# Optimization experiments

Measured on AMD Instinct MI355X. Metric: run time of the kernel, lower is better.

## Reference

```python
import jax, jax.numpy as jnp
import numpy as np

B, T, D, H, OUT = 64, 2048, 40, 164, 7


def _lstm_layer(xs, lengths, W_ih, W_hh, b):
    """xs: [T,B,Din] -> (all hiddens [T,B,H], last valid hidden [B,H]).

    Matches packed-sequence semantics: state stops updating once t >= length,
    so the final carry h equals the hidden at each sequence's last real step.
    PyTorch gate order: i, f, g, o.
    """
    Tt, Bb, _ = xs.shape
    gx = jnp.einsum('tbd,gd->tbg', xs, W_ih) + b  # input projections, one big GEMM

    def step(carry, inp):
        h, c = carry
        g_t, t = inp
        gates = g_t + h @ W_hh.T
        i, f, g, o = jnp.split(gates, 4, axis=-1)
        c_new = jax.nn.sigmoid(f) * c + jax.nn.sigmoid(i) * jnp.tanh(g)
        h_new = jax.nn.sigmoid(o) * jnp.tanh(c_new)
        m = (t < lengths)[:, None]  # freeze state past each sequence's length
        return (jnp.where(m, h_new, h), jnp.where(m, c_new, c)), jnp.where(m, h_new, h)

    z = jnp.zeros((Bb, W_hh.shape[1]), xs.dtype)
    (hT, _), hs = jax.lax.scan(step, (z, z), (gx, jnp.arange(Tt)))
    return hs, hT


def setup_inputs() -> dict:
    key = jax.random.key(0)
    ks = jax.random.split(key, 16)
    s = 1.0 / np.sqrt(H)
    inp = {
        'x': jax.random.normal(ks[0], (B, T, D), jnp.float32),
        'lengths': jax.random.randint(ks[1], (B,), 1, T + 1, jnp.int32),
        'W_ih_0': jax.random.normal(ks[2], (4 * H, D), jnp.float32) * s,
        'W_hh_0': jax.random.normal(ks[3], (4 * H, H), jnp.float32) * s,
        'b_0': jax.random.normal(ks[4], (4 * H,), jnp.float32) * s,
        'W_ih_1': jax.random.normal(ks[5], (4 * H, H), jnp.float32) * s,
        'W_hh_1': jax.random.normal(ks[6], (4 * H, H), jnp.float32) * s,
        'b_1': jax.random.normal(ks[7], (4 * H,), jnp.float32) * s,
        'W_ih_2': jax.random.normal(ks[8], (4 * H, H), jnp.float32) * s,
        'W_hh_2': jax.random.normal(ks[9], (4 * H, H), jnp.float32) * s,
        'b_2': jax.random.normal(ks[10], (4 * H,), jnp.float32) * s,
        'fc_w': jax.random.normal(ks[11], (OUT, H), jnp.float32) * s,
        'fc_b': jax.random.normal(ks[12], (OUT,), jnp.float32) * s,
    }
    return inp


def reference(x, lengths, W_ih_0, W_hh_0, b_0, W_ih_1, W_hh_1, b_1,
              W_ih_2, W_hh_2, b_2, fc_w, fc_b):
    xs = jnp.swapaxes(x, 0, 1)  # [T,B,D] for time-major scan
    hs, _ = _lstm_layer(xs, lengths, W_ih_0, W_hh_0, b_0)
    hs, _ = _lstm_layer(hs, lengths, W_ih_1, W_hh_1, b_1)
    _, hT = _lstm_layer(hs, lengths, W_ih_2, W_hh_2, b_2)  # hidden[-1]
    return hT @ fc_w.T + fc_b  # [B, OUT]
```

## Files before the change

### kernel.cpp

```cpp
#include <hip/hip_runtime.h>
#include <stdint.h>


#define TT 2048
#define BB 64
#define GG 656
#define HH 164
#define EP 176
#define GP 704
#define KPH 192
#define KPD 96
#define CC 64
#define NCH (TT/CC)
#define TSL 8
#define NSL (CC/TSL)
#define GEMM_BLKS (3*4*NSL)
#define REC_BLKS  48

typedef _Float16 half2v __attribute__((ext_vector_type(2)));
typedef _Float16 half8  __attribute__((ext_vector_type(8)));
typedef float    f32x4  __attribute__((ext_vector_type(4)));

#define SZ_WIH   ((size_t)3*GG*KPH*2)
#define SZ_WHH   ((size_t)3*GP*KPH*2)
#define SZ_GX1   ((size_t)3*16*CC*GG*4*2)
#define GX_SLOT_HALVES ((size_t)3*16*CC*GG*4)
#define SZ_HR    ((size_t)2*2*BB*CC*96*4)
#define HR_DW    (2*2*BB*CC*96)
#define SZ_SC    ((size_t)3*BB*HH*4)
#define SZ_SH    ((size_t)3*BB*96*4)

#define LOG2E 1.4426950408889634f

__device__ __forceinline__ float fexp2(float x) {
#if __has_builtin(__builtin_amdgcn_exp2f)
  return __builtin_amdgcn_exp2f(x);
#else
  float r; asm("v_exp_f32 %0, %1" : "=v"(r) : "v"(x)); return r;
#endif
}
__device__ __forceinline__ float frcp(float x) {
#if __has_builtin(__builtin_amdgcn_rcpf)
  return __builtin_amdgcn_rcpf(x);
#else
  float r; asm("v_rcp_f32 %0, %1" : "=v"(r) : "v"(x)); return r;
#endif
}
__device__ __forceinline__ float sigmf(float x) {
  return frcp(1.0f + fexp2(-LOG2E * x));
}
__device__ __forceinline__ float tanhf_(float x) {
  return __builtin_fmaf(-2.0f, frcp(1.0f + fexp2(2.0f * LOG2E * x)), 1.0f);
}

__global__ void kprep_w(const float* wih0, const float* whh0,
                        const float* wih1, const float* whh1,
                        const float* wih2, const float* whh2,
                        _Float16* wih16, _Float16* whh16) {
  int i = threadIdx.x + blockIdx.x * blockDim.x;
  if (i >= 3*GP*KPH) return;
  int l = i / (GP*KPH);
  int r2 = i - l*(GP*KPH);
  int prow = r2 / KPH;
  int k = r2 - prow*KPH;
  const float* wihl = (l == 0) ? wih0 : ((l == 1) ? wih1 : wih2);
  const float* whhl = (l == 0) ? whh0 : ((l == 1) ? whh1 : whh2);
  int g = prow / EP, e = prow - g*EP;
  float vh = 0.f;
  if (e < HH && k < HH) vh = whhl[(size_t)(g*HH + e)*HH + k];
  whh16[((size_t)l*GP + prow)*KPH + k] = (_Float16)vh;
  if (prow < GG) {
    float vi = 0.f;
    if (l == 0) { if (k < 40) vi = wihl[(size_t)prow*40 + k]; }
    else        { if (k < HH) vi = wihl[(size_t)prow*HH + k]; }
    wih16[((size_t)l*GG + prow)*KPH + k] = (_Float16)vi;
  }
}

__global__ void kzero(uint32_t* p, int n) {
  int i = threadIdx.x + blockIdx.x * blockDim.x;
  if (i < n) p[i] = 0u;
}

__device__ __forceinline__ void gemm_body(
    int l, int bg, int ts, int ch, const int* lengths, const float* x,
    const uint32_t* wihw, const uint32_t* hring, const float* bp,
    uint16_t* gxs, uint32_t* smem, int tid) {
  int maxlen = 1;
  #pragma unroll
  for (int bi = 0; bi < 16; ++bi) {
    int L = lengths[bg*16 + bi]; if (L < 1) L = 1; if (L > TT) L = TT;
    if (L > maxlen) maxlen = L;
  }
  const int tb = ts*TSL;
  const int t0 = ch*CC + tb;
  if (t0 >= maxlen) return;
  int tcnt = maxlen - t0; if (tcnt > TSL) tcnt = TSL;

  if (l == 0) {
    for (int idx = tid; idx < TSL*16*96; idx += 704) {
      int tloc = idx / 1536, r = idx - tloc*1536, b = r / 96, dw = r - b*96;
      uint32_t v = 0;
      if (dw < 20) {
        const float* xs = x + ((size_t)(bg*16 + b)*TT + (t0 + tloc))*40 + dw*2;
        half2v pp; pp[0] = (_Float16)xs[0]; pp[1] = (_Float16)xs[1];
        v = __builtin_bit_cast(uint32_t, pp);
      }
      smem[(tloc*16 + b)*100 + dw] = v;
    }
  } else {
    const uint32_t* hbs = hring + ((size_t)((l-1)*2 + (ch & 1))*BB)*CC*96;
    for (int idx = tid; idx < TSL*16*96; idx += 704) {
      int tloc = idx / 1536, r = idx - tloc*1536, b = r / 96, dw = r - b*96;
      smem[(tloc*16 + b)*100 + dw] =
          hbs[((size_t)(bg*16 + b)*CC + tb + tloc)*96 + dw];
    }
  }
  __syncthreads();

  const int lane = tid & 63, wv = tid >> 6;
  const int quad = lane >> 4, n15 = lane & 15;
  uint16_t* gxo = gxs + (((size_t)(l*16 + bg*4 + quad)*CC + tb)*GG)*4;

  half8 wf[4][6];
  float bv[4] = {0.f, 0.f, 0.f, 0.f};
  #pragma unroll
  for (int ni = 0; ni < 4; ++ni) {
    int nt = wv + ni*11;
    if (nt < 41) {
      int wrow = nt*16 + n15;
      const half8* bsrc = (const half8*)(wihw + ((size_t)l*GG + wrow)*KPD);
      #pragma unroll
      for (int kk = 0; kk < 6; ++kk) wf[ni][kk] = bsrc[kk*4 + quad];
      bv[ni] = bp[wrow];
    }
  }

  for (int tloc = 0; tloc < tcnt; ++tloc) {
    const half8* asrc = (const half8*)(smem + tloc*1600);
    half8 af[6];
    #pragma unroll
    for (int kk = 0; kk < 6; ++kk) af[kk] = asrc[n15*25 + kk*4 + quad];
    #pragma unroll
    for (int ni = 0; ni < 4; ++ni) {
      int nt = wv + ni*11;
      if (nt < 41) {
        int wrow = nt*16 + n15;
        f32x4 a0 = {0.f,0.f,0.f,0.f};
        #pragma unroll
        for (int kk = 0; kk < 6; ++kk)
          a0 = __builtin_amdgcn_mfma_f32_16x16x32_f16(af[kk], wf[ni][kk], a0, 0, 0, 0);
        half2v p0; p0[0] = (_Float16)(a0[0] + bv[ni]); p0[1] = (_Float16)(a0[1] + bv[ni]);
        half2v p1; p1[0] = (_Float16)(a0[2] + bv[ni]); p1[1] = (_Float16)(a0[3] + bv[ni]);
        uint2 pk;
        pk.x = __builtin_bit_cast(uint32_t, p0);
        pk.y = __builtin_bit_cast(uint32_t, p1);
        *(uint2*)(gxo + ((size_t)tloc*GG + wrow)*4) = pk;
      }
    }
  }
}

__device__ __forceinline__ void rec_body(
    int l, int bg, int ch, const int* lengths,
    const uint32_t* whhw, const uint16_t* gxs, uint32_t* hring,
    float* state_c, uint32_t* state_h, uint32_t* smem, int tid) {

  const int gb0 = bg*4;
  int maxlen = 1;
  #pragma unroll
  for (int bi = 0; bi < 4; ++bi) {
    int L = lengths[gb0 + bi]; if (L < 1) L = 1; if (L > TT) L = TT;
    if (L > maxlen) maxlen = L;
  }
  const int t0 = ch*CC;
  if (t0 >= maxlen) return;
  int t1 = t0 + CC; if (t1 > maxlen) t1 = maxlen;
  const int nst = t1 - t0;

  const int wv = tid >> 6, ln = tid & 63;
  const int quad = ln >> 4, n15 = ln & 15;
  const int e = wv*16 + n15;
  const int evalid = (e < HH);
  const int gb = gb0 + quad;

  int lenq = lengths[gb]; if (lenq < 1) lenq = 1; if (lenq > TT) lenq = TT;

  half8 wB[24];
  {
    const half8* wb8 = (const half8*)(whhw + (size_t)l*GP*KPD);
    #pragma unroll
    for (int g = 0; g < 4; ++g) {
      int row = g*EP + e;
      #pragma unroll
      for (int kk = 0; kk < 6; ++kk)
        wB[g*6 + kk] = wb8[(size_t)row*24 + kk*4 + quad];
    }
  }

  float creg = 0.f;
  if (ch > 0 && evalid)
    creg = state_c[((size_t)l*BB + gb)*HH + e];

  uint32_t* hb0 = smem;
  uint32_t* hb1 = smem + 1600;
  for (int i2 = tid; i2 < 1600; i2 += 704) {
    int bb = i2 / 100, dd = i2 - bb*100;
    uint32_t v = 0;
    if (dd < 96 && ch > 0) v = state_h[((size_t)l*BB + gb0 + (bb >> 2))*96 + dd];
    hb0[i2] = v; hb1[i2] = v;
  }
  __syncthreads();

  uint16_t hbit = ((const uint16_t*)hb0)[(quad*4)*200 + e];

  const uint16_t* gpt = gxs + (((size_t)(l*16 + bg)*CC)*GG)*4
                            + (size_t)e*4 + quad;
  uint16_t gxv[4];
  #pragma unroll
  for (int g = 0; g < 4; ++g) gxv[g] = gpt[g*(HH*4)];
  gpt += GG*4;

  const int dorb = (l < 2);
  uint16_t* rp;
  {
    uint16_t* hrb16 = (uint16_t*)(hring + ((size_t)(l*2 + (ch & 1))*BB)*CC*96);
    rp = hrb16 + ((size_t)gb*CC)*192 + e;
  }

  const int lo = n15*100 + quad*4;
  const int ho_off = (quad*4)*200 + e;

  int p = 0;
  for (int it = 0; it < nst; ++it) {
    const int t = t0 + it;
    uint32_t* hin  = p ? hb1 : hb0;
    uint32_t* hout = p ? hb0 : hb1;

    float gxf0 = (float)__builtin_bit_cast(_Float16, gxv[0]);
    float gxf1 = (float)__builtin_bit_cast(_Float16, gxv[1]);
    float gxf2 = (float)__builtin_bit_cast(_Float16, gxv[2]);
    float gxf3 = (float)__builtin_bit_cast(_Float16, gxv[3]);
    #pragma unroll
    for (int g = 0; g < 4; ++g) gxv[g] = gpt[g*(HH*4)];
    gpt += GG*4;

    f32x4 acc0, acc1, acc2, acc3;
    {
      const f32x4 z = {0.f, 0.f, 0.f, 0.f};
      half8 af = *(const half8*)&hin[lo];
      acc0 = __builtin_amdgcn_mfma_f32_16x16x32_f16(af, wB[0],  z, 0, 0, 0);
      acc1 = __builtin_amdgcn_mfma_f32_16x16x32_f16(af, wB[6],  z, 0, 0, 0);
      acc2 = __builtin_amdgcn_mfma_f32_16x16x32_f16(af, wB[12], z, 0, 0, 0);
      acc3 = __builtin_amdgcn_mfma_f32_16x16x32_f16(af, wB[18], z, 0, 0, 0);
    }
    #pragma unroll
    for (int kk = 1; kk < 6; ++kk) {
      half8 af = *(const half8*)&hin[lo + kk*16];
      acc0 = __builtin_amdgcn_mfma_f32_16x16x32_f16(af, wB[kk],      acc0, 0, 0, 0);
      acc1 = __builtin_amdgcn_mfma_f32_16x16x32_f16(af, wB[6 + kk],  acc1, 0, 0, 0);
      acc2 = __builtin_amdgcn_mfma_f32_16x16x32_f16(af, wB[12 + kk], acc2, 0, 0, 0);
      acc3 = __builtin_amdgcn_mfma_f32_16x16x32_f16(af, wB[18 + kk], acc3, 0, 0, 0);
    }
    {
      float gi = acc0[0] + gxf0;
      float gf = acc1[0] + gxf1;
      float gg2 = acc2[0] + gxf2;
      float go = acc3[0] + gxf3;
      float cn = sigmf(gf)*creg + sigmf(gi)*tanhf_(gg2);
      float hv = sigmf(go)*tanhf_(cn);
      if (t < lenq) {
        creg = cn;
        _Float16 h16 = (_Float16)hv;
        hbit = __builtin_bit_cast(uint16_t, h16);
      }
      if (evalid) {
        ((uint16_t*)hout)[ho_off] = hbit;
        if (dorb) *rp = hbit;
      }
      rp += 192;
    }
    asm volatile("s_waitcnt lgkmcnt(0)" ::: "memory");
    __builtin_amdgcn_s_barrier();
    p ^= 1;
  }

  uint32_t* hfin = p ? hb1 : hb0;
  uint32_t* shb = state_h + ((size_t)l*BB + gb0)*96;
  for (int i2 = tid; i2 < 4*96; i2 += 704) {
    int bb = i2 / 96, dd = i2 - bb*96;
    shb[(size_t)bb*96 + dd] = hfin[(bb*4)*100 + dd];
  }
  if (evalid)
    state_c[((size_t)l*BB + gb)*HH + e] = creg;
}

__global__ __launch_bounds__(704, 1) void kstep_f(
    int j, const int* lengths, const float* x,
    const uint32_t* wihw, const uint32_t* whhw,
    const float* b0, const float* b1, const float* b2,
    uint16_t* gx, uint32_t* hring, float* state_c, uint32_t* state_h) {
  __shared__ __align__(16) uint32_t smem[TSL*1600];
  const int blk = blockIdx.x, tid = threadIdx.x;
  if (blk < GEMM_BLKS) {
    const int l = blk / (4*NSL);
    const int r = blk - l*(4*NSL);
    const int bg = r / NSL, ts = r - bg*NSL;
    const int ch = j - 2*l;
    if (ch < 0 || ch >= NCH) return;
    const float* bp = (l == 0) ? b0 : ((l == 1) ? b1 : b2);
    uint16_t* gxs = gx + (size_t)(ch & 1)*GX_SLOT_HALVES;
    gemm_body(l, bg, ts, ch, lengths, x, wihw, hring, bp, gxs, smem, tid);
  } else {
    const int idx = blk - GEMM_BLKS;
    if (idx >= REC_BLKS) return;
    const int l = idx >> 4, bg = idx & 15;
    const int ch = j - 2*l - 1;
    if (ch < 0 || ch >= NCH) return;
    const uint16_t* gxs = gx + (size_t)(ch & 1)*GX_SLOT_HALVES;
    rec_body(l, bg, ch, lengths, whhw, gxs, hring,
             state_c, state_h, smem, tid);
  }
}

__global__ __launch_bounds__(704, 1) void kgemm_s(
    int step, const int* lengths, const float* x,
    const uint32_t* wihw, const float* b0, const float* b1, const float* b2,
    uint16_t* gx, const uint32_t* hring) {
  __shared__ __align__(16) uint32_t smem[TSL*1600];
  const int blk = blockIdx.x;
  const int l = blk / (4*NSL);
  const int r = blk - l*(4*NSL);
  const int bg = r / NSL, ts = r - bg*NSL;
  const int ch = step - l;
  if (ch < 0 || ch >= NCH) return;
  const float* bp = (l == 0) ? b0 : ((l == 1) ? b1 : b2);
  gemm_body(l, bg, ts, ch, lengths, x, wihw, hring, bp, gx, smem, threadIdx.x);
}

__global__ __launch_bounds__(704, 1) void krec_s(
    int step, const int* lengths,
    const uint32_t* whhw, const uint16_t* gx, uint32_t* hring,
    float* state_c, uint32_t* state_h) {
  __shared__ __align__(16) uint32_t smem[TSL*1600];
  const int idx = blockIdx.x;
  const int l = idx >> 4, bg = idx & 15;
  const int ch = step - l;
  if (ch < 0 || ch >= NCH) return;
  rec_body(l, bg, ch, lengths, whhw, gx, hring,
           state_c, state_h, smem, threadIdx.x);
}

__global__ void kfc(const float* fcw, const float* fcb,
                    const uint32_t* state_h, float* out) {
  int b = blockIdx.x, o = threadIdx.x;
  if (o >= 7) return;
  const uint16_t* h16 = (const uint16_t*)(state_h + (size_t)(2*BB + b)*96);
  float s = fcb[o];
  for (int m = 0; m < HH; ++m) {
    _Float16 hv = __builtin_bit_cast(_Float16, h16[m]);
    s += fcw[o*HH + m] * (float)hv;
  }
  out[b*7 + o] = s;
}

extern "C" void kernel_launch(void* const* d_in, const int* in_sizes, int n_in,
                              void* d_out, int out_size, void* d_ws, size_t ws_size,
                              hipStream_t stream) {
  const float* x      = (const float*)d_in[0];
  const int*  lengths = (const int*)  d_in[1];
  const float* wih0   = (const float*)d_in[2];
  const float* whh0   = (const float*)d_in[3];
  const float* b0     = (const float*)d_in[4];
  const float* wih1   = (const float*)d_in[5];
  const float* whh1   = (const float*)d_in[6];
  const float* b1     = (const float*)d_in[7];
  const float* wih2   = (const float*)d_in[8];
  const float* whh2   = (const float*)d_in[9];
  const float* b2     = (const float*)d_in[10];
  const float* fcw    = (const float*)d_in[11];
  const float* fcb    = (const float*)d_in[12];

  const size_t off_wih = 0;
  const size_t off_whh = SZ_WIH;
  const size_t off_gx  = SZ_WIH + SZ_WHH;
  const size_t tail    = SZ_HR + SZ_SC + SZ_SH;
  const size_t need_fused = off_gx + 2*SZ_GX1 + tail;
  const size_t need_seq   = off_gx + 1*SZ_GX1 + tail;
  const int fused = (ws_size >= need_fused);
  if (!fused && ws_size < need_seq) return;
  const size_t gx_bytes = fused ? 2*SZ_GX1 : SZ_GX1;
  const size_t off_hr = off_gx + gx_bytes;
  const size_t off_sc = off_hr + SZ_HR;
  const size_t off_sh = off_sc + SZ_SC;

  char* ws = (char*)d_ws;
  _Float16* wih16 = (_Float16*)(ws + off_wih);
  _Float16* whh16 = (_Float16*)(ws + off_whh);
  uint16_t* gxw   = (uint16_t*)(ws + off_gx);
  uint32_t* hrw   = (uint32_t*)(ws + off_hr);
  float*    scw   = (float*)   (ws + off_sc);
  uint32_t* shw   = (uint32_t*)(ws + off_sh);

  hipLaunchKernelGGL(kprep_w, dim3((3*GP*KPH + 255)/256), dim3(256), 0, stream,
                     wih0, whh0, wih1, whh1, wih2, whh2, wih16, whh16);
  hipLaunchKernelGGL(kzero, dim3((HR_DW + 255)/256), dim3(256), 0, stream,
                     hrw, HR_DW);

  if (fused) {
    for (int jj = 0; jj <= NCH + 4; ++jj) {
      hipLaunchKernelGGL(kstep_f, dim3(GEMM_BLKS + REC_BLKS), dim3(704), 0,
                         stream, jj, lengths, x, (const uint32_t*)wih16,
                         (const uint32_t*)whh16, b0, b1, b2,
                         gxw, hrw, scw, shw);
    }
  } else {
    for (int i = 0; i < NCH + 2; ++i) {
      hipLaunchKernelGGL(kgemm_s, dim3(GEMM_BLKS), dim3(704), 0, stream,
                         i, lengths, x, (const uint32_t*)wih16,
                         b0, b1, b2, gxw, (const uint32_t*)hrw);
      hipLaunchKernelGGL(krec_s, dim3(REC_BLKS), dim3(704), 0, stream,
                         i, lengths, (const uint32_t*)whh16,
                         (const uint16_t*)gxw, hrw, scw, shw);
    }
  }

  hipLaunchKernelGGL(kfc, dim3(64), dim3(64), 0, stream,
                     fcw, fcb, shw, (float*)d_out);
}
```

Measured before the change: 2.296 ms.

## Replace per-chunk kernel launches with one persistent cooperative kernel using grid sync

Adds a persistent cooperative kernel that loops over all chunk steps internally, using grid.sync between steps instead of launching kstep_f once per chunk. GEMM blocks keep their input-weight fragments and biases in registers across steps, and recurrent blocks keep their W_hh fragments, c state and h buffers resident rather than reloading them and spilling state to global memory each launch. This removes launch overhead and per-launch state save and restore. In exchange it needs all 144 blocks co-resident and pays a grid-wide barrier with fences each step; if the cooperative launch fails, it falls back to the old per-chunk path.

```diff
diff --git a/kernel.cpp b/kernel.cpp
--- a/kernel.cpp
+++ b/kernel.cpp
@@ -1,4 +1,5 @@
 #include <hip/hip_runtime.h>
+#include <hip/hip_cooperative_groups.h>
 #include <stdint.h>
 
 
@@ -16,6 +17,7 @@
 #define NSL (CC/TSL)
 #define GEMM_BLKS (3*4*NSL)
 #define REC_BLKS  48
+#define NBLK_COOP (GEMM_BLKS + REC_BLKS)
 
 typedef _Float16 half2v __attribute__((ext_vector_type(2)));
 typedef _Float16 half8  __attribute__((ext_vector_type(8)));
@@ -293,6 +295,220 @@
   }
   if (evalid)
     state_c[((size_t)l*BB + gb)*HH + e] = creg;
+}
+
+__global__ __launch_bounds__(704, 1) void kstep_coop(
+    const int* lengths, const float* x,
+    const uint32_t* wihw, const uint32_t* whhw,
+    const float* b0, const float* b1, const float* b2,
+    uint16_t* gx, uint32_t* hring, uint32_t* state_h) {
+  cooperative_groups::grid_group grid = cooperative_groups::this_grid();
+  __shared__ __align__(16) uint32_t smem[TSL*1600];
+  const int blk = blockIdx.x, tid = threadIdx.x;
+
+  if (blk < GEMM_BLKS) {
+    const int l = blk / (4*NSL);
+    const int r = blk - l*(4*NSL);
+    const int bg = r / NSL, ts = r - bg*NSL;
+    const int tb = ts*TSL;
+    int maxlen = 1;
+    #pragma unroll
+    for (int bi = 0; bi < 16; ++bi) {
+      int L = lengths[bg*16 + bi]; if (L < 1) L = 1; if (L > TT) L = TT;
+      if (L > maxlen) maxlen = L;
+    }
+    const int lane = tid & 63, wv = tid >> 6;
+    const int quad = lane >> 4, n15 = lane & 15;
+    const float* bp = (l == 0) ? b0 : ((l == 1) ? b1 : b2);
+
+    half8 wf[4][6];
+    float bv[4] = {0.f, 0.f, 0.f, 0.f};
+    #pragma unroll
+    for (int ni = 0; ni < 4; ++ni) {
+      int nt = wv + ni*11;
+      if (nt < 41) {
+        int wrow = nt*16 + n15;
+        const half8* bsrc = (const half8*)(wihw + ((size_t)l*GG + wrow)*KPD);
+        #pragma unroll
+        for (int kk = 0; kk < 6; ++kk) wf[ni][kk] = bsrc[kk*4 + quad];
+        bv[ni] = bp[wrow];
+      }
+    }
+
+    for (int j = 0; j <= NCH + 4; ++j) {
+      const int ch = j - 2*l;
+      if (ch >= 0 && ch < NCH) {
+        const int t0 = ch*CC + tb;
+        if (t0 < maxlen) {
+          int tcnt = maxlen - t0; if (tcnt > TSL) tcnt = TSL;
+          uint16_t* gxs = gx + (size_t)(ch & 1)*GX_SLOT_HALVES;
+          if (l == 0) {
+            for (int idx = tid; idx < TSL*16*96; idx += 704) {
+              int tloc = idx / 1536, rr = idx - tloc*1536, b = rr / 96, dw = rr - b*96;
+              uint32_t v = 0;
+              if (dw < 20) {
+                const float* xs = x + ((size_t)(bg*16 + b)*TT + (t0 + tloc))*40 + dw*2;
+                half2v pp; pp[0] = (_Float16)xs[0]; pp[1] = (_Float16)xs[1];
+                v = __builtin_bit_cast(uint32_t, pp);
+              }
+              smem[(tloc*16 + b)*100 + dw] = v;
+            }
+          } else {
+            const uint32_t* hbs = hring + ((size_t)((l-1)*2 + (ch & 1))*BB)*CC*96;
+            for (int idx = tid; idx < TSL*16*96; idx += 704) {
+              int tloc = idx / 1536, rr = idx - tloc*1536, b = rr / 96, dw = rr - b*96;
+              smem[(tloc*16 + b)*100 + dw] =
+                  hbs[((size_t)(bg*16 + b)*CC + tb + tloc)*96 + dw];
+            }
+          }
+          __syncthreads();
+          uint16_t* gxo = gxs + (((size_t)(l*16 + bg*4 + quad)*CC + tb)*GG)*4;
+          for (int tloc = 0; tloc < tcnt; ++tloc) {
+            const half8* asrc = (const half8*)(smem + tloc*1600);
+            half8 af[6];
+            #pragma unroll
+            for (int kk = 0; kk < 6; ++kk) af[kk] = asrc[n15*25 + kk*4 + quad];
+            #pragma unroll
+            for (int ni = 0; ni < 4; ++ni) {
+              int nt = wv + ni*11;
+              if (nt < 41) {
+                int wrow = nt*16 + n15;
+                f32x4 a0 = {0.f,0.f,0.f,0.f};
+                #pragma unroll
+                for (int kk = 0; kk < 6; ++kk)
+                  a0 = __builtin_amdgcn_mfma_f32_16x16x32_f16(af[kk], wf[ni][kk], a0, 0, 0, 0);
+                half2v p0; p0[0] = (_Float16)(a0[0] + bv[ni]); p0[1] = (_Float16)(a0[1] + bv[ni]);
+                half2v p1; p1[0] = (_Float16)(a0[2] + bv[ni]); p1[1] = (_Float16)(a0[3] + bv[ni]);
+                uint2 pk;
+                pk.x = __builtin_bit_cast(uint32_t, p0);
+                pk.y = __builtin_bit_cast(uint32_t, p1);
+                *(uint2*)(gxo + ((size_t)tloc*GG + wrow)*4) = pk;
+              }
+            }
+          }
+        }
+      }
+      __threadfence();
+      grid.sync();
+    }
+  } else {
+    const int idx0 = blk - GEMM_BLKS;
+    const int l = idx0 >> 4, bg = idx0 & 15;
+    const int gb0 = bg*4;
+    int maxlen = 1;
+    #pragma unroll
+    for (int bi = 0; bi < 4; ++bi) {
+      int L = lengths[gb0 + bi]; if (L < 1) L = 1; if (L > TT) L = TT;
+      if (L > maxlen) maxlen = L;
+    }
+    const int wv = tid >> 6, ln = tid & 63;
+    const int quad = ln >> 4, n15 = ln & 15;
+    const int e = wv*16 + n15;
+    const int evalid = (e < HH);
+    const int gb = gb0 + quad;
+    int lenq = lengths[gb]; if (lenq < 1) lenq = 1; if (lenq > TT) lenq = TT;
+
+    half8 wB[24];
+    {
+      const half8* wb8 = (const half8*)(whhw + (size_t)l*GP*KPD);
+      #pragma unroll
+      for (int g = 0; g < 4; ++g) {
+        int row = g*EP + e;
+        #pragma unroll
+        for (int kk = 0; kk < 6; ++kk)
+          wB[g*6 + kk] = wb8[(size_t)row*24 + kk*4 + quad];
+      }
+    }
+    float creg = 0.f;
+    uint16_t hbit = 0;
+    uint32_t* hb0 = smem;
+    uint32_t* hb1 = smem + 1600;
+    for (int i2 = tid; i2 < 1600; i2 += 704) { hb0[i2] = 0u; hb1[i2] = 0u; }
+    __syncthreads();
+
+    const int lo = n15*100 + quad*4;
+    const int ho_off = (quad*4)*200 + e;
+    const int dorb = (l < 2);
+    int p = 0;
+
+    for (int j = 0; j <= NCH + 4; ++j) {
+      const int ch = j - 2*l - 1;
+      if (ch >= 0 && ch < NCH && ch*CC < maxlen) {
+        const int t0 = ch*CC;
+        int t1 = t0 + CC; if (t1 > maxlen) t1 = maxlen;
+        const uint16_t* gxs = gx + (size_t)(ch & 1)*GX_SLOT_HALVES;
+        const uint16_t* gpt = gxs + (((size_t)(l*16 + bg)*CC)*GG)*4
+                                  + (size_t)e*4 + quad;
+        uint16_t gxv[4];
+        #pragma unroll
+        for (int g = 0; g < 4; ++g) gxv[g] = gpt[g*(HH*4)];
+        gpt += GG*4;
+        uint16_t* rp = (uint16_t*)(hring + ((size_t)(l*2 + (ch & 1))*BB)*CC*96)
+                       + ((size_t)gb*CC)*192 + e;
+
+        for (int t = t0; t < t1; ++t) {
+          uint32_t* hin  = p ? hb1 : hb0;
+          uint32_t* hout = p ? hb0 : hb1;
+
+          float gxf0 = (float)__builtin_bit_cast(_Float16, gxv[0]);
+          float gxf1 = (float)__builtin_bit_cast(_Float16, gxv[1]);
+          float gxf2 = (float)__builtin_bit_cast(_Float16, gxv[2]);
+          float gxf3 = (float)__builtin_bit_cast(_Float16, gxv[3]);
+          #pragma unroll
+          for (int g = 0; g < 4; ++g) gxv[g] = gpt[g*(HH*4)];
+          gpt += GG*4;
+
+          f32x4 acc0, acc1, acc2, acc3;
+          {
+            const f32x4 z = {0.f, 0.f, 0.f, 0.f};
+            half8 af = *(const half8*)&hin[lo];
+            acc0 = __builtin_amdgcn_mfma_f32_16x16x32_f16(af, wB[0],  z, 0, 0, 0);
+            acc1 = __builtin_amdgcn_mfma_f32_16x16x32_f16(af, wB[6],  z, 0, 0, 0);
+            acc2 = __builtin_amdgcn_mfma_f32_16x16x32_f16(af, wB[12], z, 0, 0, 0);
+            acc3 = __builtin_amdgcn_mfma_f32_16x16x32_f16(af, wB[18], z, 0, 0, 0);
+          }
+          #pragma unroll
+          for (int kk = 1; kk < 6; ++kk) {
+            half8 af = *(const half8*)&hin[lo + kk*16];
+            acc0 = __builtin_amdgcn_mfma_f32_16x16x32_f16(af, wB[kk],      acc0, 0, 0, 0);
+            acc1 = __builtin_amdgcn_mfma_f32_16x16x32_f16(af, wB[6 + kk],  acc1, 0, 0, 0);
+            acc2 = __builtin_amdgcn_mfma_f32_16x16x32_f16(af, wB[12 + kk], acc2, 0, 0, 0);
+            acc3 = __builtin_amdgcn_mfma_f32_16x16x32_f16(af, wB[18 + kk], acc3, 0, 0, 0);
+          }
+          {
+            float gi = acc0[0] + gxf0;
+            float gf = acc1[0] + gxf1;
+            float gg2 = acc2[0] + gxf2;
+            float go = acc3[0] + gxf3;
+            float cn = sigmf(gf)*creg + sigmf(gi)*tanhf_(gg2);
+            float hv = sigmf(go)*tanhf_(cn);
+            if (t < lenq) {
+              creg = cn;
+              _Float16 h16 = (_Float16)hv;
+              hbit = __builtin_bit_cast(uint16_t, h16);
+            }
+            if (evalid) {
+              ((uint16_t*)hout)[ho_off] = hbit;
+              if (dorb) *rp = hbit;
+            }
+            rp += 192;
+          }
+          asm volatile("s_waitcnt lgkmcnt(0)" ::: "memory");
+          __builtin_amdgcn_s_barrier();
+          p ^= 1;
+        }
+      }
+      __threadfence();
+      grid.sync();
+    }
+
+    uint32_t* hfin = p ? hb1 : hb0;
+    uint32_t* shb = state_h + ((size_t)l*BB + gb0)*96;
+    for (int i2 = tid; i2 < 4*96; i2 += 704) {
+      int bb = i2 / 96, dd = i2 - bb*96;
+      shb[(size_t)bb*96 + dd] = hfin[(bb*4)*100 + dd];
+    }
+  }
 }
 
 __global__ __launch_bounds__(704, 1) void kstep_f(
@@ -407,14 +623,29 @@
   hipLaunchKernelGGL(kzero, dim3((HR_DW + 255)/256), dim3(256), 0, stream,
                      hrw, HR_DW);
 
+  int done = 0;
   if (fused) {
+    const uint32_t* wihc = (const uint32_t*)wih16;
+    const uint32_t* whhc = (const uint32_t*)whh16;
+    void* kargs[] = {
+      (void*)&lengths, (void*)&x, (void*)&wihc, (void*)&whhc,
+      (void*)&b0, (void*)&b1, (void*)&b2,
+      (void*)&gxw, (void*)&hrw, (void*)&shw
+    };
+    hipError_t err = hipLaunchCooperativeKernel(
+        (const void*)kstep_coop, dim3(NBLK_COOP), dim3(704), kargs, 0, stream);
+    if (err == hipSuccess) done = 1;
+  }
+  if (!done && fused) {
     for (int jj = 0; jj <= NCH + 4; ++jj) {
-      hipLaunchKernelGGL(kstep_f, dim3(GEMM_BLKS + REC_BLKS), dim3(704), 0,
+      hipLaunchKernelGGL(kstep_f, dim3(NBLK_COOP), dim3(704), 0,
                          stream, jj, lengths, x, (const uint32_t*)wih16,
                          (const uint32_t*)whh16, b0, b1, b2,
                          gxw, hrw, scw, shw);
     }
-  } else {
+    done = 1;
+  }
+  if (!done) {
     for (int i = 0; i < NCH + 2; ++i) {
       hipLaunchKernelGGL(kgemm_s, dim3(GEMM_BLKS), dim3(704), 0, stream,
                          i, lengths, x, (const uint32_t*)wih16,
```

Result: slower. 3.842 ms (+67.3%).
